# Kernel optimization log

Hardware: AMD Instinct MI355X
Metric: run time of the kernel (lower is better)

## Reference

```python
import jax, jax.numpy as jnp
import numpy as np

T, B, M = 2048, 256, 32


def setup_inputs() -> dict:
    key = jax.random.key(0)
    k1, k2, k3, k4 = jax.random.split(key, 4)
    emissions = jax.random.normal(k1, (T, B, M), jnp.float32)
    tags = jax.random.randint(k2, (T, B), 0, M)
    # weight divides transition scores -> keep strictly positive
    weight = jax.random.uniform(k3, (T, B), jnp.float32, 0.5, 1.5)
    mask = jnp.ones((T, B), jnp.int32)  # first timestep must be all-on
    transitions = jax.random.normal(k4, (M, M), jnp.float32) * 0.1
    start_transitions = jnp.zeros((M,), jnp.float32)
    end_transitions = jnp.zeros((M,), jnp.float32)
    return {
        "emissions": emissions,
        "tags": tags,
        "weight": weight,
        "mask": mask,
        "transitions": transitions,
        "start_transitions": start_transitions,
        "end_transitions": end_transitions,
    }


def reference(emissions, tags, weight, mask, transitions, start_transitions, end_transitions):
    # emissions: [T,B,M]; tags/weight/mask: [T,B]; reduction='sum' (torch default)
    Tn, Bn, Mn = emissions.shape
    maskb = mask.astype(bool)
    tags = jnp.where(maskb, tags, 1)
    maskf = mask.astype(emissions.dtype)

    # ---- gold-path score (_compute_score) ----
    score = start_transitions[tags[0]]
    score = score + (transitions[tags[:-1], tags[1:]] * maskf[1:] / weight[:-1]).sum(0)
    em_sc = jnp.take_along_axis(emissions, tags[:, :, None], axis=-1)[..., 0] * maskf
    score = score + em_sc.sum(0)
    seq_ends = mask.astype(jnp.int32).sum(0) - 1  # [B]
    last_tags = tags[seq_ends, jnp.arange(Bn)]
    score = score + end_transitions[last_tags]

    # ---- log-partition (_compute_normalizer) via logsumexp-semiring scan ----
    neg_inf = jnp.asarray(-jnp.inf, emissions.dtype)
    log_eye = jnp.where(jnp.eye(Mn, dtype=bool), jnp.zeros((), emissions.dtype), neg_inf)

    alpha0 = start_transitions + emissions[0]  # [B,M]

    def step(alpha, xs):
        em_t, w_t, m_t = xs  # [B,M], [B], [B]
        sc = transitions[None, :, :] / w_t[:, None, None] + em_t[:, None, :]  # [B,M,M]
        sc = jnp.where(m_t[:, None, None], sc, log_eye)  # masked step = identity in log-semiring
        alpha = jax.nn.logsumexp(alpha[:, :, None] + sc, axis=1)
        return alpha, None

    alpha, _ = jax.lax.scan(step, alpha0, (emissions[1:], weight[:-1], maskb[1:]))
    log_Z = jax.nn.logsumexp(alpha + end_transitions, axis=1)  # [B]

    nllh = log_Z - score
    return nllh.sum()
```

## Files before the change

### kernel.cpp

```cpp
#include <hip/hip_runtime.h>
#include <hip/hip_bf16.h>
#include <stdint.h>


#define T_DIM 2048
#define B_DIM 256
#define M_DIM 32
#define CHUNKS 32
#define CLEN 64
#define NBLK ((CHUNKS * B_DIM) / 16)
#define KSC 184.6649652337873f
#define SBIAS2 12599160.66f

typedef __attribute__((ext_vector_type(8))) short short8;
typedef __attribute__((ext_vector_type(16))) float f32x16;
typedef __attribute__((ext_vector_type(2))) float f32x2;

__device__ __forceinline__ int pack_bf16(float lo, float hi) {
  union { float f; uint32_t u; } a, b;
  a.f = lo; b.f = hi;
  return (int)__builtin_amdgcn_perm(b.u, a.u, 0x07060302u);
}

__device__ __forceinline__ int pack_lo16(int lo, int hi) {
  return (int)__builtin_amdgcn_perm((uint32_t)hi, (uint32_t)lo, 0x05040100u);
}

__device__ __forceinline__ float bcast_lane(float v, int idx) {
  return __int_as_float(__builtin_amdgcn_readlane(__float_as_int(v), idx));
}

__global__ __launch_bounds__(256, 2) void chunk_kernel(
    const float* __restrict__ em, const int* __restrict__ tags,
    const float* __restrict__ wt, const int* __restrict__ mask,
    const float* __restrict__ trans, const float* __restrict__ endt,
    uint32_t* __restrict__ mats, float* __restrict__ offs,
    float* __restrict__ scoreP, uint32_t* __restrict__ ctrl)
{
  int tid = threadIdx.x;
  if (tid == 0) ctrl[0] = 0;
  int lane = tid & 63;
  int h = lane >> 5;
  int r = lane & 31;
  int wid = blockIdx.x * 4 + (tid >> 6);
  int u0 = 4 * wid;
  int bb = u0 & (B_DIM - 1);
  int c = u0 >> 8;
  int t0 = 1 + c * CLEN;
  int t1 = t0 + CLEN; if (t1 > T_DIM) t1 = T_DIM;

  f32x2 tp2[8];
#pragma unroll
  for (int u = 0; u < 4; ++u) {
    int j0 = 2 * u, j1 = 2 * u + 1;
    int row0 = ((j0 < 4) ? j0 : j0 + 4) + 4 * h;
    int row1 = ((j1 < 4) ? j1 : j1 + 4) + 4 * h;
    tp2[u][0]     = trans[row0 * 32 + r] * KSC;
    tp2[u][1]     = trans[row1 * 32 + r] * KSC;
    tp2[4 + u][0] = trans[(row0 + 16) * 32 + r] * KSC;
    tp2[4 + u][1] = trans[(row1 + 16) * 32 + r] * KSC;
  }

  int tw = t0 - 1 + lane; if (tw > T_DIM - 1) tw = T_DIM - 1;
  int tmk = t0 + lane; if (tmk > T_DIM - 1) tmk = T_DIM - 1;
  float rwv[4];
  uint64_t mk[4];
  uint64_t valid = (t1 - t0 >= 64) ? ~0ull : ((1ull << (t1 - t0)) - 1ull);
#pragma unroll
  for (int ch = 0; ch < 4; ++ch) {
    rwv[ch] = __builtin_amdgcn_rcpf(wt[tw * B_DIM + bb + ch]);
    mk[ch] = __ballot(mask[tmk * B_DIM + bb + ch] != 0) & valid;
  }

  f32x16 X[4];
#pragma unroll
  for (int p = 0; p < 16; ++p) {
    float v = (((p & 3) + 8 * (p >> 2) + 4 * h) == r) ? 1.f : 0.f;
    X[0][p] = v; X[1][p] = v; X[2][p] = v; X[3][p] = v;
  }
  f32x16 z;
#pragma unroll
  for (int u = 0; u < 16; ++u) z[u] = 0.f;

  float off2[4] = {0.f, 0.f, 0.f, 0.f};

  auto step4 = [&](const float* e4, int s) {
    float rw0 = bcast_lane(rwv[0], s), rw1 = bcast_lane(rwv[1], s);
    float rw2 = bcast_lane(rwv[2], s), rw3 = bcast_lane(rwv[3], s);
    float rw[4] = {rw0, rw1, rw2, rw3};
    union { int i[4]; short8 s8; } af1[4], af2[4], b1[4], b2[4];
#pragma unroll
    for (int ch = 0; ch < 4; ++ch) {
      float e = fmaf(e4[ch], KSC, SBIAS2);
      f32x2 e2 = {e, e}, rwp = {rw[ch], rw[ch]};
#pragma unroll
      for (int u = 0; u < 4; ++u) {
        union { f32x2 v; int i[2]; } qa, qb;
        qa.v = __builtin_elementwise_fma(tp2[u],     rwp, e2);
        qb.v = __builtin_elementwise_fma(tp2[4 + u], rwp, e2);
        af1[ch].i[u] = pack_lo16(qa.i[0], qa.i[1]);
        af2[ch].i[u] = pack_lo16(qb.i[0], qb.i[1]);
      }
    }
#pragma unroll
    for (int ch = 0; ch < 4; ++ch)
#pragma unroll
      for (int u = 0; u < 4; ++u) {
        b1[ch].i[u] = pack_bf16(X[ch][2 * u],     X[ch][2 * u + 1]);
        b2[ch].i[u] = pack_bf16(X[ch][8 + 2 * u], X[ch][8 + 2 * u + 1]);
      }
    f32x16 d[4];
#pragma unroll
    for (int ch = 0; ch < 4; ++ch)
      d[ch] = __builtin_amdgcn_mfma_f32_32x32x16_bf16(af1[ch].s8, b1[ch].s8, z, 0, 0, 0);
#pragma unroll
    for (int ch = 0; ch < 4; ++ch)
      X[ch] = __builtin_amdgcn_mfma_f32_32x32x16_bf16(af2[ch].s8, b2[ch].s8, d[ch], 0, 0, 0);
  };

  auto stepOne = [&](f32x16& Xc, float e_em, float rw) {
    float e = fmaf(e_em, KSC, SBIAS2);
    f32x2 e2 = {e, e}, rwp = {rw, rw};
    union { int i[4]; short8 s8; } af1, af2, b1_, b2_;
#pragma unroll
    for (int u = 0; u < 4; ++u) {
      union { f32x2 v; int i[2]; } qa, qb;
      qa.v = __builtin_elementwise_fma(tp2[u],     rwp, e2);
      qb.v = __builtin_elementwise_fma(tp2[4 + u], rwp, e2);
      af1.i[u] = pack_lo16(qa.i[0], qa.i[1]);
      af2.i[u] = pack_lo16(qb.i[0], qb.i[1]);
      b1_.i[u] = pack_bf16(Xc[2 * u],     Xc[2 * u + 1]);
      b2_.i[u] = pack_bf16(Xc[8 + 2 * u], Xc[8 + 2 * u + 1]);
    }
    f32x16 d = __builtin_amdgcn_mfma_f32_32x32x16_bf16(af1.s8, b1_.s8, z, 0, 0, 0);
    Xc = __builtin_amdgcn_mfma_f32_32x32x16_bf16(af2.s8, b2_.s8, d, 0, 0, 0);
  };

  auto rescale = [&](f32x16& Xc, float& o2) {
    float mx = Xc[0];
#pragma unroll
    for (int u = 1; u < 16; ++u) mx = fmaxf(mx, Xc[u]);
#pragma unroll
    for (int off = 1; off < 64; off <<= 1) mx = fmaxf(mx, __shfl_xor(mx, off));
    float sc = __builtin_amdgcn_rcpf(mx);
    o2 += __builtin_amdgcn_logf(mx);
#pragma unroll
    for (int u = 0; u < 16; ++u) Xc[u] *= sc;
  };

  bool fast = (t1 - t0 == 64) && (mk[0] == ~0ull) && (mk[1] == ~0ull)
            && (mk[2] == ~0ull) && (mk[3] == ~0ull);

  if (fast) {
    float e[4][4], n[4][4];
#pragma unroll
    for (int ch = 0; ch < 4; ++ch)
#pragma unroll
      for (int u = 0; u < 4; ++u)
        e[ch][u] = em[((size_t)((t0 + 2 * u + h) * B_DIM + bb + ch)) * 32 + r];
    for (int g = 0; g < 8; ++g) {
      int tg = t0 + 8 * (g + 1);
#pragma unroll
      for (int ch = 0; ch < 4; ++ch)
#pragma unroll
        for (int u = 0; u < 4; ++u) {
          int tt = tg + 2 * u + h; if (tt > T_DIM - 1) tt = T_DIM - 1;
          n[ch][u] = em[((size_t)(tt * B_DIM + bb + ch)) * 32 + r];
        }
#pragma unroll
      for (int u = 0; u < 4; ++u) {
        int sA = 8 * g + 2 * u, sB = sA + 1;
        float eA[4], eB[4];
#pragma unroll
        for (int ch = 0; ch < 4; ++ch) {
          float sw = __shfl_xor(e[ch][u], 32);
          eA[ch] = h ? sw : e[ch][u];
          eB[ch] = h ? e[ch][u] : sw;
        }
        step4(eA, sA);
        step4(eB, sB);
      }
#pragma unroll
      for (int ch = 0; ch < 4; ++ch) rescale(X[ch], off2[ch]);
#pragma unroll
      for (int ch = 0; ch < 4; ++ch)
#pragma unroll
        for (int u = 0; u < 4; ++u) e[ch][u] = n[ch][u];
    }
  } else {
    float emv[4], emp[4];
#pragma unroll
    for (int ch = 0; ch < 4; ++ch)
      emv[ch] = em[((size_t)((t0 + h) * B_DIM + bb + ch)) * 32 + r];
    int tpf = t0 + 2 + h; if (tpf > T_DIM - 1) tpf = T_DIM - 1;
#pragma unroll
    for (int ch = 0; ch < 4; ++ch)
      emp[ch] = em[((size_t)(tpf * B_DIM + bb + ch)) * 32 + r];

    for (int it = 0; it < CLEN / 2; ++it) {
      int tn = t0 + 2 * it + 4 + h; if (tn > T_DIM - 1) tn = T_DIM - 1;
      float emn[4];
#pragma unroll
      for (int ch = 0; ch < 4; ++ch)
        emn[ch] = em[((size_t)(tn * B_DIM + bb + ch)) * 32 + r];

      int sA = 2 * it, sB = sA + 1;
#pragma unroll
      for (int ch = 0; ch < 4; ++ch) {
        float sw = __shfl_xor(emv[ch], 32);
        if ((mk[ch] >> sA) & 1)
          stepOne(X[ch], h ? sw : emv[ch], bcast_lane(rwv[ch], sA));
        if ((t0 + sB < t1) && ((mk[ch] >> sB) & 1))
          stepOne(X[ch], h ? emv[ch] : sw, bcast_lane(rwv[ch], sB));
      }

      if ((it & 3) == 3) {
#pragma unroll
        for (int ch = 0; ch < 4; ++ch) rescale(X[ch], off2[ch]);
      }
#pragma unroll
      for (int ch = 0; ch < 4; ++ch) { emv[ch] = emp[ch]; emp[ch] = emn[ch]; }
    }
  }

#pragma unroll
  for (int ch = 0; ch < 4; ++ch) {
    uint32_t* mp = mats + (size_t)(u0 + ch) * 512;
#pragma unroll
    for (int u = 0; u < 8; ++u) {
      int pairIdx = (u & 1) + (u >> 1) * 4 + 2 * h;
      mp[pairIdx * 32 + r] = (uint32_t)pack_bf16(X[ch][2 * u], X[ch][2 * u + 1]);
    }
  }
  if (lane == 0) {
#pragma unroll
    for (int ch = 0; ch < 4; ++ch) offs[u0 + ch] = off2[ch];
  }

  int t = t0 + lane;
  float ssc = 0.f;
  if (t < t1) {
#pragma unroll
    for (int ch = 0; ch < 4; ++ch) {
      int b = bb + ch;
      int mkc  = mask[t * B_DIM + b];
      int mkn  = (t + 1 < T_DIM) ? mask[(t + 1) * B_DIM + b] : 0;
      int tg   = mkc ? tags[t * B_DIM + b] : 1;
      int mkp  = mask[(t - 1) * B_DIM + b];
      int tgp  = mkp ? tags[(t - 1) * B_DIM + b] : 1;
      if (mkc)
        ssc += em[(size_t)(t * B_DIM + b) * 32 + tg]
             + trans[tgp * 32 + tg] * __builtin_amdgcn_rcpf(wt[(t - 1) * B_DIM + b]);
      if (mkc && !mkn) ssc += endt[tg];
    }
  }
#pragma unroll
  for (int off = 32; off; off >>= 1) ssc += __shfl_xor(ssc, off);
  if (lane == 0) scoreP[wid] = -ssc;
}

__global__ __launch_bounds__(256, 1) void combine_kernel(
    const float* __restrict__ em, const int* __restrict__ tags,
    const int* __restrict__ mask, const float* __restrict__ startt,
    const float* __restrict__ endt, const uint32_t* __restrict__ mats,
    const float* __restrict__ offs, const float* __restrict__ scoreP,
    float* __restrict__ res, uint32_t* __restrict__ ctrl,
    float* __restrict__ out)
{
  const float INV_LN2 = 1.44269504088896340736f;
  const float LN2 = 0.69314718055994530942f;
  __shared__ float Plds[4][32][36];
  __shared__ float logw[4];

  int tid = threadIdx.x;
  int lane = tid & 63;
  int w = tid >> 6;
  int r = lane & 31;
  int h = lane >> 5;
  int b = blockIdx.x;

  uint32_t rsel = (r & 1) ? 0x07060302u : 0x05040100u;
  int rowoff = (r >> 1) * 32;

  f32x16 P, z;
#pragma unroll
  for (int p = 0; p < 16; ++p) {
    P[p] = ((((p & 3) + 8 * (p >> 2) + 4 * h) == r) ? 1.f : 0.f);
    z[p] = 0.f;
  }

  int c0 = 8 * w;
  uint4 L[4][4];
#pragma unroll
  for (int i = 0; i < 4; ++i) {
    const uint4* mb = (const uint4*)(mats + ((size_t)(c0 + i) * B_DIM + b) * 512 + rowoff);
    L[i][0] = mb[h]; L[i][1] = mb[2 + h]; L[i][2] = mb[4 + h]; L[i][3] = mb[6 + h];
  }

  float lw = 0.f;
#pragma unroll
  for (int i = 0; i < 8; ++i) {
    uint4 A0 = L[i & 3][0], A1 = L[i & 3][1], A2 = L[i & 3][2], A3 = L[i & 3][3];
    if (i + 4 < 8) {
      const uint4* mb = (const uint4*)(mats + ((size_t)(c0 + i + 4) * B_DIM + b) * 512 + rowoff);
      L[i & 3][0] = mb[h]; L[i & 3][1] = mb[2 + h];
      L[i & 3][2] = mb[4 + h]; L[i & 3][3] = mb[6 + h];
    }
    union { int i4[4]; short8 s8; } af1, af2, b1, b2;
    af1.i4[0] = (int)__builtin_amdgcn_perm(A0.y, A0.x, rsel);
    af1.i4[1] = (int)__builtin_amdgcn_perm(A0.w, A0.z, rsel);
    af1.i4[2] = (int)__builtin_amdgcn_perm(A1.y, A1.x, rsel);
    af1.i4[3] = (int)__builtin_amdgcn_perm(A1.w, A1.z, rsel);
    af2.i4[0] = (int)__builtin_amdgcn_perm(A2.y, A2.x, rsel);
    af2.i4[1] = (int)__builtin_amdgcn_perm(A2.w, A2.z, rsel);
    af2.i4[2] = (int)__builtin_amdgcn_perm(A3.y, A3.x, rsel);
    af2.i4[3] = (int)__builtin_amdgcn_perm(A3.w, A3.z, rsel);
#pragma unroll
    for (int u = 0; u < 4; ++u) {
      b1.i4[u] = pack_bf16(P[2 * u],     P[2 * u + 1]);
      b2.i4[u] = pack_bf16(P[8 + 2 * u], P[8 + 2 * u + 1]);
    }
    f32x16 d = __builtin_amdgcn_mfma_f32_32x32x16_bf16(af1.s8, b1.s8, z, 0, 0, 0);
    P = __builtin_amdgcn_mfma_f32_32x32x16_bf16(af2.s8, b2.s8, d, 0, 0, 0);
    lw += offs[(size_t)(c0 + i) * B_DIM + b];
  }

  float mx = P[0];
#pragma unroll
  for (int p = 1; p < 16; ++p) mx = fmaxf(mx, P[p]);
#pragma unroll
  for (int off = 1; off < 64; off <<= 1) mx = fmaxf(mx, __shfl_xor(mx, off));
  float sc = __builtin_amdgcn_rcpf(mx);
  lw += __builtin_amdgcn_logf(mx);
#pragma unroll
  for (int p = 0; p < 16; ++p)
    Plds[w][(p & 3) + 8 * (p >> 2) + 4 * h][r] = P[p] * sc;
  if (lane == 0) logw[w] = lw;
  __syncthreads();

  if (tid >= 64) return;

  int j = r;
  float a0 = (startt[j] + em[(size_t)b * 32 + j]) * INV_LN2;
  float cm = a0;
#pragma unroll
  for (int off = 1; off < 32; off <<= 1) cm = fmaxf(cm, __shfl_xor(cm, off));
  float av = __builtin_amdgcn_exp2f(a0 - cm);
  float acc = cm + logw[0] + logw[1] + logw[2] + logw[3];

#pragma unroll
  for (int wv = 0; wv < 4; ++wv) {
    const float4* Pr = (const float4*)&Plds[wv][j][16 * h];
    float4 q0 = Pr[0], q1 = Pr[1], q2 = Pr[2], q3 = Pr[3];
    int cb = 16 * h;
    float s = fmaf(q0.x, __shfl(av, cb + 0),
              fmaf(q0.y, __shfl(av, cb + 1),
              fmaf(q0.z, __shfl(av, cb + 2),
                   q0.w * __shfl(av, cb + 3))));
    s = fmaf(q1.x, __shfl(av, cb + 4),
        fmaf(q1.y, __shfl(av, cb + 5),
        fmaf(q1.z, __shfl(av, cb + 6),
        fmaf(q1.w, __shfl(av, cb + 7), s))));
    s = fmaf(q2.x, __shfl(av, cb + 8),
        fmaf(q2.y, __shfl(av, cb + 9),
        fmaf(q2.z, __shfl(av, cb + 10),
        fmaf(q2.w, __shfl(av, cb + 11), s))));
    s = fmaf(q3.x, __shfl(av, cb + 12),
        fmaf(q3.y, __shfl(av, cb + 13),
        fmaf(q3.z, __shfl(av, cb + 14),
        fmaf(q3.w, __shfl(av, cb + 15), s))));
    float an = s + __shfl_xor(s, 32);
    float m2 = an;
#pragma unroll
    for (int off = 1; off < 32; off <<= 1) m2 = fmaxf(m2, __shfl_xor(m2, off));
    av = an * __builtin_amdgcn_rcpf(m2);
    acc += __builtin_amdgcn_logf(m2);
  }

  float sv = av * __builtin_amdgcn_exp2f(endt[j] * INV_LN2);
#pragma unroll
  for (int off = 1; off < 32; off <<= 1) sv += __shfl_xor(sv, off);
  if (lane == 0) {
    float logZ = (acc + __builtin_amdgcn_logf(sv)) * LN2;
    int mk0 = mask[b];
    int tg0 = mk0 ? tags[b] : 1;
    float s0 = startt[tg0] + (mk0 ? em[(size_t)b * 32 + tg0] : 0.f);
    int mk1 = mask[B_DIM + b];
    if (mk0 && !mk1) s0 += endt[tg0];
    res[b] = logZ - s0;
  }

  __builtin_amdgcn_fence(__ATOMIC_RELEASE, "agent");
  unsigned old = 0;
  if (lane == 0) old = atomicAdd(&ctrl[0], 1u);
  old = (unsigned)__shfl((int)old, 0);
  if (old == (unsigned)(B_DIM - 1)) {
    __builtin_amdgcn_fence(__ATOMIC_ACQUIRE, "agent");
    float s = 0.f;
#pragma unroll
    for (int i = 0; i < 4; ++i) s += res[lane + 64 * i];
#pragma unroll
    for (int i = 0; i < 32; ++i) s += scoreP[lane + 64 * i];
#pragma unroll
    for (int off = 32; off; off >>= 1) s += __shfl_xor(s, off);
    if (lane == 0) out[0] = s;
  }
}

extern "C" void kernel_launch(void* const* d_in, const int* in_sizes, int n_in,
                              void* d_out, int out_size, void* d_ws, size_t ws_size,
                              hipStream_t stream) {
  const float* em   = (const float*)d_in[0];
  const int*   tags = (const int*)d_in[1];
  const float* wt   = (const float*)d_in[2];
  const int*   mask = (const int*)d_in[3];
  const float* tr   = (const float*)d_in[4];
  const float* stt  = (const float*)d_in[5];
  const float* ent  = (const float*)d_in[6];
  float* out = (float*)d_out;

  uint32_t* ctrl  = (uint32_t*)d_ws;
  float* res      = (float*)d_ws + 4;
  float* scoreP   = res + B_DIM;
  float* offs     = scoreP + 4 * NBLK;
  uint32_t* mats  = (uint32_t*)(offs + CHUNKS * B_DIM);

  chunk_kernel<<<NBLK, 256, 0, stream>>>(em, tags, wt, mask, tr, ent,
                                         mats, offs, scoreP, ctrl);
  combine_kernel<<<B_DIM, 256, 0, stream>>>(em, tags, mask, stt, ent,
                                            mats, offs, scoreP, res, ctrl, out);
}
```

Measured before the change: 167.3 us.

## Fuse chunk and combine kernels into one per-batch block using LDS

Merges the chunked transfer-matrix kernel and the combine kernel into a single kernel with one 512-thread block per batch element, where each of 8 waves handles 4 consecutive chunks of that sequence. Chunk matrices and offsets are kept in LDS instead of round-tripping through global workspace, and the gold-path score is reduced inside the block. This removes the intermediate global writes/reads and the second kernel's dependency, but now uses only 256 blocks of 512 threads, and each wave's emission loads for its 4 chunks are strided far apart in time rather than across adjacent batch entries. A tiny zero kernel replaces the in-kernel counter reset.

Result: no change. 168.6 us (+0.8%).

```diff
diff --git a/kernel.cpp b/kernel.cpp
--- a/kernel.cpp
+++ b/kernel.cpp
@@ -8,7 +8,6 @@
 #define M_DIM 32
 #define CHUNKS 32
 #define CLEN 64
-#define NBLK ((CHUNKS * B_DIM) / 16)
 #define KSC 184.6649652337873f
 #define SBIAS2 12599160.66f
 
@@ -30,24 +29,30 @@
   return __int_as_float(__builtin_amdgcn_readlane(__float_as_int(v), idx));
 }
 
-__global__ __launch_bounds__(256, 2) void chunk_kernel(
+__global__ void zero_kernel(uint32_t* __restrict__ ctrl) {
+  if (threadIdx.x == 0) ctrl[0] = 0;
+}
+
+__global__ __launch_bounds__(512, 1) void crf_kernel(
     const float* __restrict__ em, const int* __restrict__ tags,
     const float* __restrict__ wt, const int* __restrict__ mask,
-    const float* __restrict__ trans, const float* __restrict__ endt,
-    uint32_t* __restrict__ mats, float* __restrict__ offs,
-    float* __restrict__ scoreP, uint32_t* __restrict__ ctrl)
+    const float* __restrict__ trans, const float* __restrict__ startt,
+    const float* __restrict__ endt, float* __restrict__ res,
+    uint32_t* __restrict__ ctrl, float* __restrict__ out)
 {
+  const float INV_LN2 = 1.44269504088896340736f;
+  const float LN2 = 0.69314718055994530942f;
+  __shared__ __align__(16) uint32_t matsL[CHUNKS][16][36];
+  __shared__ __align__(16) float PL[8][32][36];
+  __shared__ float logw[8];
+  __shared__ float scoreW[8];
+
   int tid = threadIdx.x;
-  if (tid == 0) ctrl[0] = 0;
   int lane = tid & 63;
+  int w = tid >> 6;
   int h = lane >> 5;
   int r = lane & 31;
-  int wid = blockIdx.x * 4 + (tid >> 6);
-  int u0 = 4 * wid;
-  int bb = u0 & (B_DIM - 1);
-  int c = u0 >> 8;
-  int t0 = 1 + c * CLEN;
-  int t1 = t0 + CLEN; if (t1 > T_DIM) t1 = T_DIM;
+  int b = blockIdx.x;
 
   f32x2 tp2[8];
 #pragma unroll
@@ -61,27 +66,29 @@
     tp2[4 + u][1] = trans[(row1 + 16) * 32 + r] * KSC;
   }
 
-  int tw = t0 - 1 + lane; if (tw > T_DIM - 1) tw = T_DIM - 1;
-  int tmk = t0 + lane; if (tmk > T_DIM - 1) tmk = T_DIM - 1;
+  int t0c[4], lenc[4];
   float rwv[4];
   uint64_t mk[4];
-  uint64_t valid = (t1 - t0 >= 64) ? ~0ull : ((1ull << (t1 - t0)) - 1ull);
 #pragma unroll
   for (int ch = 0; ch < 4; ++ch) {
-    rwv[ch] = __builtin_amdgcn_rcpf(wt[tw * B_DIM + bb + ch]);
-    mk[ch] = __ballot(mask[tmk * B_DIM + bb + ch] != 0) & valid;
-  }
-
-  f32x16 X[4];
+    int c = 4 * w + ch;
+    t0c[ch] = 1 + c * CLEN;
+    int t1 = t0c[ch] + CLEN; if (t1 > T_DIM) t1 = T_DIM;
+    lenc[ch] = t1 - t0c[ch];
+    int tw = t0c[ch] - 1 + lane; if (tw > T_DIM - 1) tw = T_DIM - 1;
+    int tm = t0c[ch] + lane;     if (tm > T_DIM - 1) tm = T_DIM - 1;
+    rwv[ch] = __builtin_amdgcn_rcpf(wt[tw * B_DIM + b]);
+    uint64_t valid = (lenc[ch] >= 64) ? ~0ull : ((1ull << lenc[ch]) - 1ull);
+    mk[ch] = __ballot(mask[tm * B_DIM + b] != 0) & valid;
+  }
+
+  f32x16 X[4], z;
 #pragma unroll
   for (int p = 0; p < 16; ++p) {
     float v = (((p & 3) + 8 * (p >> 2) + 4 * h) == r) ? 1.f : 0.f;
     X[0][p] = v; X[1][p] = v; X[2][p] = v; X[3][p] = v;
-  }
-  f32x16 z;
-#pragma unroll
-  for (int u = 0; u < 16; ++u) z[u] = 0.f;
-
+    z[p] = 0.f;
+  }
   float off2[4] = {0.f, 0.f, 0.f, 0.f};
 
   auto step4 = [&](const float* e4, int s) {
@@ -148,24 +155,36 @@
     for (int u = 0; u < 16; ++u) Xc[u] *= sc;
   };
 
-  bool fast = (t1 - t0 == 64) && (mk[0] == ~0ull) && (mk[1] == ~0ull)
-            && (mk[2] == ~0ull) && (mk[3] == ~0ull);
-
-  if (fast) {
+  int minLen = lenc[0];
+  if (lenc[1] < minLen) minLen = lenc[1];
+  if (lenc[2] < minLen) minLen = lenc[2];
+  if (lenc[3] < minLen) minLen = lenc[3];
+  int Gc = minLen >> 3;
+  bool allFull = true;
+#pragma unroll
+  for (int ch = 0; ch < 4; ++ch) {
+    uint64_t need = (8 * Gc >= 64) ? ~0ull : ((1ull << (8 * Gc)) - 1ull);
+    allFull = allFull && ((mk[ch] & need) == need);
+  }
+  int G = allFull ? Gc : 0;
+
+  if (G > 0) {
     float e[4][4], n[4][4];
 #pragma unroll
     for (int ch = 0; ch < 4; ++ch)
 #pragma unroll
-      for (int u = 0; u < 4; ++u)
-        e[ch][u] = em[((size_t)((t0 + 2 * u + h) * B_DIM + bb + ch)) * 32 + r];
-    for (int g = 0; g < 8; ++g) {
-      int tg = t0 + 8 * (g + 1);
+      for (int u = 0; u < 4; ++u) {
+        int tt = t0c[ch] + 2 * u + h; if (tt > T_DIM - 1) tt = T_DIM - 1;
+        e[ch][u] = em[((size_t)(tt * B_DIM + b)) * 32 + r];
+      }
+    for (int g = 0; g < G; ++g) {
 #pragma unroll
       for (int ch = 0; ch < 4; ++ch)
 #pragma unroll
         for (int u = 0; u < 4; ++u) {
-          int tt = tg + 2 * u + h; if (tt > T_DIM - 1) tt = T_DIM - 1;
-          n[ch][u] = em[((size_t)(tt * B_DIM + bb + ch)) * 32 + r];
+          int tt = t0c[ch] + 8 * (g + 1) + 2 * u + h;
+          if (tt > T_DIM - 1) tt = T_DIM - 1;
+          n[ch][u] = em[((size_t)(tt * B_DIM + b)) * 32 + r];
         }
 #pragma unroll
       for (int u = 0; u < 4; ++u) {
@@ -187,33 +206,33 @@
 #pragma unroll
         for (int u = 0; u < 4; ++u) e[ch][u] = n[ch][u];
     }
-  } else {
+  }
+  if (G < 8) {
+    int s0 = 8 * G;
     float emv[4], emp[4];
 #pragma unroll
-    for (int ch = 0; ch < 4; ++ch)
-      emv[ch] = em[((size_t)((t0 + h) * B_DIM + bb + ch)) * 32 + r];
-    int tpf = t0 + 2 + h; if (tpf > T_DIM - 1) tpf = T_DIM - 1;
-#pragma unroll
-    for (int ch = 0; ch < 4; ++ch)
-      emp[ch] = em[((size_t)(tpf * B_DIM + bb + ch)) * 32 + r];
-
-    for (int it = 0; it < CLEN / 2; ++it) {
-      int tn = t0 + 2 * it + 4 + h; if (tn > T_DIM - 1) tn = T_DIM - 1;
+    for (int ch = 0; ch < 4; ++ch) {
+      int tv = t0c[ch] + s0 + h;     if (tv > T_DIM - 1) tv = T_DIM - 1;
+      int tp = t0c[ch] + s0 + 2 + h; if (tp > T_DIM - 1) tp = T_DIM - 1;
+      emv[ch] = em[((size_t)(tv * B_DIM + b)) * 32 + r];
+      emp[ch] = em[((size_t)(tp * B_DIM + b)) * 32 + r];
+    }
+    for (int it = 4 * G; it < CLEN / 2; ++it) {
       float emn[4];
 #pragma unroll
-      for (int ch = 0; ch < 4; ++ch)
-        emn[ch] = em[((size_t)(tn * B_DIM + bb + ch)) * 32 + r];
-
+      for (int ch = 0; ch < 4; ++ch) {
+        int tn = t0c[ch] + 2 * it + 4 + h; if (tn > T_DIM - 1) tn = T_DIM - 1;
+        emn[ch] = em[((size_t)(tn * B_DIM + b)) * 32 + r];
+      }
       int sA = 2 * it, sB = sA + 1;
 #pragma unroll
       for (int ch = 0; ch < 4; ++ch) {
         float sw = __shfl_xor(emv[ch], 32);
         if ((mk[ch] >> sA) & 1)
           stepOne(X[ch], h ? sw : emv[ch], bcast_lane(rwv[ch], sA));
-        if ((t0 + sB < t1) && ((mk[ch] >> sB) & 1))
+        if ((mk[ch] >> sB) & 1)
           stepOne(X[ch], h ? emv[ch] : sw, bcast_lane(rwv[ch], sB));
       }
-
       if ((it & 3) == 3) {
 #pragma unroll
         for (int ch = 0; ch < 4; ++ch) rescale(X[ch], off2[ch]);
@@ -225,29 +244,24 @@
 
 #pragma unroll
   for (int ch = 0; ch < 4; ++ch) {
-    uint32_t* mp = mats + (size_t)(u0 + ch) * 512;
+    int c = 4 * w + ch;
 #pragma unroll
     for (int u = 0; u < 8; ++u) {
       int pairIdx = (u & 1) + (u >> 1) * 4 + 2 * h;
-      mp[pairIdx * 32 + r] = (uint32_t)pack_bf16(X[ch][2 * u], X[ch][2 * u + 1]);
-    }
-  }
-  if (lane == 0) {
-#pragma unroll
-    for (int ch = 0; ch < 4; ++ch) offs[u0 + ch] = off2[ch];
-  }
-
-  int t = t0 + lane;
+      matsL[c][pairIdx][r] = (uint32_t)pack_bf16(X[ch][2 * u], X[ch][2 * u + 1]);
+    }
+  }
+
   float ssc = 0.f;
-  if (t < t1) {
-#pragma unroll
-    for (int ch = 0; ch < 4; ++ch) {
-      int b = bb + ch;
-      int mkc  = mask[t * B_DIM + b];
-      int mkn  = (t + 1 < T_DIM) ? mask[(t + 1) * B_DIM + b] : 0;
-      int tg   = mkc ? tags[t * B_DIM + b] : 1;
-      int mkp  = mask[(t - 1) * B_DIM + b];
-      int tgp  = mkp ? tags[(t - 1) * B_DIM + b] : 1;
+#pragma unroll
+  for (int k = 0; k < 4; ++k) {
+    int t = 1 + tid + 512 * k;
+    if (t < T_DIM) {
+      int mkc = mask[t * B_DIM + b];
+      int mkn = (t + 1 < T_DIM) ? mask[(t + 1) * B_DIM + b] : 0;
+      int tg  = mkc ? tags[t * B_DIM + b] : 1;
+      int mkp = mask[(t - 1) * B_DIM + b];
+      int tgp = mkp ? tags[(t - 1) * B_DIM + b] : 1;
       if (mkc)
         ssc += em[(size_t)(t * B_DIM + b) * 32 + tg]
              + trans[tgp * 32 + tg] * __builtin_amdgcn_rcpf(wt[(t - 1) * B_DIM + b]);
@@ -256,86 +270,52 @@
   }
 #pragma unroll
   for (int off = 32; off; off >>= 1) ssc += __shfl_xor(ssc, off);
-  if (lane == 0) scoreP[wid] = -ssc;
-}
-
-__global__ __launch_bounds__(256, 1) void combine_kernel(
-    const float* __restrict__ em, const int* __restrict__ tags,
-    const int* __restrict__ mask, const float* __restrict__ startt,
-    const float* __restrict__ endt, const uint32_t* __restrict__ mats,
-    const float* __restrict__ offs, const float* __restrict__ scoreP,
-    float* __restrict__ res, uint32_t* __restrict__ ctrl,
-    float* __restrict__ out)
-{
-  const float INV_LN2 = 1.44269504088896340736f;
-  const float LN2 = 0.69314718055994530942f;
-  __shared__ float Plds[4][32][36];
-  __shared__ float logw[4];
-
-  int tid = threadIdx.x;
-  int lane = tid & 63;
-  int w = tid >> 6;
-  int r = lane & 31;
-  int h = lane >> 5;
-  int b = blockIdx.x;
-
-  uint32_t rsel = (r & 1) ? 0x07060302u : 0x05040100u;
-  int rowoff = (r >> 1) * 32;
-
-  f32x16 P, z;
-#pragma unroll
-  for (int p = 0; p < 16; ++p) {
-    P[p] = ((((p & 3) + 8 * (p >> 2) + 4 * h) == r) ? 1.f : 0.f);
-    z[p] = 0.f;
-  }
-
-  int c0 = 8 * w;
-  uint4 L[4][4];
-#pragma unroll
-  for (int i = 0; i < 4; ++i) {
-    const uint4* mb = (const uint4*)(mats + ((size_t)(c0 + i) * B_DIM + b) * 512 + rowoff);
-    L[i][0] = mb[h]; L[i][1] = mb[2 + h]; L[i][2] = mb[4 + h]; L[i][3] = mb[6 + h];
-  }
-
-  float lw = 0.f;
-#pragma unroll
-  for (int i = 0; i < 8; ++i) {
-    uint4 A0 = L[i & 3][0], A1 = L[i & 3][1], A2 = L[i & 3][2], A3 = L[i & 3][3];
-    if (i + 4 < 8) {
-      const uint4* mb = (const uint4*)(mats + ((size_t)(c0 + i + 4) * B_DIM + b) * 512 + rowoff);
-      L[i & 3][0] = mb[h]; L[i & 3][1] = mb[2 + h];
-      L[i & 3][2] = mb[4 + h]; L[i & 3][3] = mb[6 + h];
-    }
-    union { int i4[4]; short8 s8; } af1, af2, b1, b2;
-    af1.i4[0] = (int)__builtin_amdgcn_perm(A0.y, A0.x, rsel);
-    af1.i4[1] = (int)__builtin_amdgcn_perm(A0.w, A0.z, rsel);
-    af1.i4[2] = (int)__builtin_amdgcn_perm(A1.y, A1.x, rsel);
-    af1.i4[3] = (int)__builtin_amdgcn_perm(A1.w, A1.z, rsel);
-    af2.i4[0] = (int)__builtin_amdgcn_perm(A2.y, A2.x, rsel);
-    af2.i4[1] = (int)__builtin_amdgcn_perm(A2.w, A2.z, rsel);
-    af2.i4[2] = (int)__builtin_amdgcn_perm(A3.y, A3.x, rsel);
-    af2.i4[3] = (int)__builtin_amdgcn_perm(A3.w, A3.z, rsel);
-#pragma unroll
-    for (int u = 0; u < 4; ++u) {
-      b1.i4[u] = pack_bf16(P[2 * u],     P[2 * u + 1]);
-      b2.i4[u] = pack_bf16(P[8 + 2 * u], P[8 + 2 * u + 1]);
-    }
-    f32x16 d = __builtin_amdgcn_mfma_f32_32x32x16_bf16(af1.s8, b1.s8, z, 0, 0, 0);
-    P = __builtin_amdgcn_mfma_f32_32x32x16_bf16(af2.s8, b2.s8, d, 0, 0, 0);
-    lw += offs[(size_t)(c0 + i) * B_DIM + b];
-  }
-
-  float mx = P[0];
-#pragma unroll
-  for (int p = 1; p < 16; ++p) mx = fmaxf(mx, P[p]);
-#pragma unroll
-  for (int off = 1; off < 64; off <<= 1) mx = fmaxf(mx, __shfl_xor(mx, off));
-  float sc = __builtin_amdgcn_rcpf(mx);
-  lw += __builtin_amdgcn_logf(mx);
-#pragma unroll
-  for (int p = 0; p < 16; ++p)
-    Plds[w][(p & 3) + 8 * (p >> 2) + 4 * h][r] = P[p] * sc;
-  if (lane == 0) logw[w] = lw;
+  if (lane == 0) scoreW[w] = ssc;
+
+  __syncthreads();
+
+  {
+    uint32_t rsel = (r & 1) ? 0x07060302u : 0x05040100u;
+    f32x16 P;
+#pragma unroll
+    for (int p = 0; p < 16; ++p)
+      P[p] = ((((p & 3) + 8 * (p >> 2) + 4 * h) == r) ? 1.f : 0.f);
+    float lw = off2[0] + off2[1] + off2[2] + off2[3];
+
+#pragma unroll
+    for (int i = 0; i < 4; ++i) {
+      const uint4* mb = (const uint4*)(&matsL[4 * w + i][r >> 1][0]);
+      uint4 A0 = mb[h], A1 = mb[2 + h], A2 = mb[4 + h], A3 = mb[6 + h];
+      union { int i4[4]; short8 s8; } af1, af2, b1, b2;
+      af1.i4[0] = (int)__builtin_amdgcn_perm(A0.y, A0.x, rsel);
+      af1.i4[1] = (int)__builtin_amdgcn_perm(A0.w, A0.z, rsel);
+      af1.i4[2] = (int)__builtin_amdgcn_perm(A1.y, A1.x, rsel);
+      af1.i4[3] = (int)__builtin_amdgcn_perm(A1.w, A1.z, rsel);
+      af2.i4[0] = (int)__builtin_amdgcn_perm(A2.y, A2.x, rsel);
+      af2.i4[1] = (int)__builtin_amdgcn_perm(A2.w, A2.z, rsel);
+      af2.i4[2] = (int)__builtin_amdgcn_perm(A3.y, A3.x, rsel);
+      af2.i4[3] = (int)__builtin_amdgcn_perm(A3.w, A3.z, rsel);
+#pragma unroll
+      for (int u = 0; u < 4; ++u) {
+        b1.i4[u] = pack_bf16(P[2 * u],     P[2 * u + 1]);
+        b2.i4[u] = pack_bf16(P[8 + 2 * u], P[8 + 2 * u + 1]);
+      }
+      f32x16 d = __builtin_amdgcn_mfma_f32_32x32x16_bf16(af1.s8, b1.s8, z, 0, 0, 0);
+      P = __builtin_amdgcn_mfma_f32_32x32x16_bf16(af2.s8, b2.s8, d, 0, 0, 0);
+    }
+
+    float mx = P[0];
+#pragma unroll
+    for (int p = 1; p < 16; ++p) mx = fmaxf(mx, P[p]);
+#pragma unroll
+    for (int off = 1; off < 64; off <<= 1) mx = fmaxf(mx, __shfl_xor(mx, off));
+    float sc = __builtin_amdgcn_rcpf(mx);
+    lw += __builtin_amdgcn_logf(mx);
+#pragma unroll
+    for (int p = 0; p < 16; ++p)
+      PL[w][(p & 3) + 8 * (p >> 2) + 4 * h][r] = P[p] * sc;
+    if (lane == 0) logw[w] = lw;
+  }
   __syncthreads();
 
   if (tid >= 64) return;
@@ -346,11 +326,12 @@
 #pragma unroll
   for (int off = 1; off < 32; off <<= 1) cm = fmaxf(cm, __shfl_xor(cm, off));
   float av = __builtin_amdgcn_exp2f(a0 - cm);
-  float acc = cm + logw[0] + logw[1] + logw[2] + logw[3];
-
-#pragma unroll
-  for (int wv = 0; wv < 4; ++wv) {
-    const float4* Pr = (const float4*)&Plds[wv][j][16 * h];
+  float acc = cm + logw[0] + logw[1] + logw[2] + logw[3]
+                 + logw[4] + logw[5] + logw[6] + logw[7];
+
+#pragma unroll
+  for (int wv = 0; wv < 8; ++wv) {
+    const float4* Pr = (const float4*)&PL[wv][j][16 * h];
     float4 q0 = Pr[0], q1 = Pr[1], q2 = Pr[2], q3 = Pr[3];
     int cb = 16 * h;
     float s = fmaf(q0.x, __shfl(av, cb + 0),
@@ -387,7 +368,9 @@
     float s0 = startt[tg0] + (mk0 ? em[(size_t)b * 32 + tg0] : 0.f);
     int mk1 = mask[B_DIM + b];
     if (mk0 && !mk1) s0 += endt[tg0];
-    res[b] = logZ - s0;
+    float st = scoreW[0] + scoreW[1] + scoreW[2] + scoreW[3]
+             + scoreW[4] + scoreW[5] + scoreW[6] + scoreW[7];
+    res[b] = logZ - s0 - st;
   }
 
   __builtin_amdgcn_fence(__ATOMIC_RELEASE, "agent");
@@ -398,9 +381,7 @@
     __builtin_amdgcn_fence(__ATOMIC_ACQUIRE, "agent");
     float s = 0.f;
 #pragma unroll
-    for (int i = 0; i < 4; ++i) s += res[lane + 64 * i];
-#pragma unroll
-    for (int i = 0; i < 32; ++i) s += scoreP[lane + 64 * i];
+    for (int k = 0; k < 4; ++k) s += res[lane + 64 * k];
 #pragma unroll
     for (int off = 32; off; off >>= 1) s += __shfl_xor(s, off);
     if (lane == 0) out[0] = s;
@@ -419,14 +400,10 @@
   const float* ent  = (const float*)d_in[6];
   float* out = (float*)d_out;
 
-  uint32_t* ctrl  = (uint32_t*)d_ws;
-  float* res      = (float*)d_ws + 4;
-  float* scoreP   = res + B_DIM;
-  float* offs     = scoreP + 4 * NBLK;
-  uint32_t* mats  = (uint32_t*)(offs + CHUNKS * B_DIM);
-
-  chunk_kernel<<<NBLK, 256, 0, stream>>>(em, tags, wt, mask, tr, ent,
-                                         mats, offs, scoreP, ctrl);
-  combine_kernel<<<B_DIM, 256, 0, stream>>>(em, tags, mask, stt, ent,
-                                            mats, offs, scoreP, res, ctrl, out);
-}
+  uint32_t* ctrl = (uint32_t*)d_ws;
+  float* res     = (float*)d_ws + 4;
+
+  zero_kernel<<<1, 64, 0, stream>>>(ctrl);
+  crf_kernel<<<B_DIM, 512, 0, stream>>>(em, tags, wt, mask, tr, stt, ent,
+                                        res, ctrl, out);
+}
```
